# Performance work log

Measured on AMD Instinct MI355X. Metric: run time of the kernel, lower is better.

## Reference

```python
import jax, jax.numpy as jnp
import numpy as np

B, T, C, H = 2, 2048, 1024, 16
D = C // H  # head dim = 64
EPS = 1e-6  # kernel adds 1e-6 to softmax denominator


def setup_inputs() -> dict:
    key = jax.random.key(0)
    k1, k2, k3, k4, k5 = jax.random.split(key, 5)
    s = 1.0 / np.sqrt(C)
    return {
        "x": jax.random.normal(k1, (B, T, C), dtype=jnp.float32),
        "w_attn": jax.random.normal(k2, (3 * C, C), dtype=jnp.float32) * s,
        "b_attn": jax.random.normal(k3, (3 * C,), dtype=jnp.float32) * 0.02,
        "w_proj": jax.random.normal(k4, (C, C), dtype=jnp.float32) * s,
        "b_proj": jax.random.normal(k5, (C,), dtype=jnp.float32) * 0.02,
    }


def reference(x, w_attn, b_attn, w_proj, b_proj):
    b, t, c = x.shape
    qkv = x @ w_attn.T + b_attn                      # [B,T,3C]
    q, k, v = jnp.split(qkv, 3, axis=2)
    # [B,T,C] -> [B,H,T,D]
    q = q.reshape(b, t, H, D).transpose(0, 2, 1, 3)
    k = k.reshape(b, t, H, D).transpose(0, 2, 1, 3)
    v = v.reshape(b, t, H, D).transpose(0, 2, 1, 3)
    scale = 1.0 / np.sqrt(D)
    att = jnp.einsum("bhid,bhjd->bhij", q, k) * scale  # [B,H,T,T]
    causal = jnp.tril(jnp.ones((t, t), dtype=bool))
    att = jnp.where(causal, att, -jnp.inf)
    # softmax matching the HIP kernel: denom has +1e-6
    m = jnp.max(att, axis=-1, keepdims=True)
    e = jnp.exp(att - m)                             # masked entries -> 0
    p = e / (jnp.sum(e, axis=-1, keepdims=True) + EPS)
    y = jnp.einsum("bhij,bhjd->bhid", p, v)          # [B,H,T,D]
    y = y.transpose(0, 2, 1, 3).reshape(b, t, c)     # [B,T,C]
    return y @ w_proj.T + b_proj
```

## Files before the change

kernel.cpp:

```cpp
#include <hip/hip_runtime.h>

#define B_ 2
#define T_ 2048
#define C_ 1024
#define H_ 16
#define D_ 64

typedef __bf16 bf16x8 __attribute__((ext_vector_type(8)));
typedef float f32x4 __attribute__((ext_vector_type(4)));

__device__ __forceinline__ unsigned short f2bf(float f) {
  unsigned u = __float_as_uint(f);
  unsigned r = (u + 0x7fffu + ((u >> 16) & 1u)) >> 16;
  return (unsigned short)r;
}

#define NX 1048576
#define NWA 786432
#define NWP 262144
__global__ __launch_bounds__(256) void convert_all(
    const float* __restrict__ x, const float* __restrict__ wa,
    const float* __restrict__ wp, unsigned short* __restrict__ xb,
    unsigned short* __restrict__ wab, unsigned short* __restrict__ wpb) {
  int i = blockIdx.x * 256 + threadIdx.x;
  const float* s; unsigned short* d; int j;
  if (i < NX)            { s = x;  d = xb;  j = i; }
  else if (i < NX + NWA) { s = wa; d = wab; j = i - NX; }
  else                   { s = wp; d = wpb; j = i - NX - NWA; }
  float4 v = ((const float4*)s)[j];
  ushort4 u;
  u.x = f2bf(v.x); u.y = f2bf(v.y); u.z = f2bf(v.z); u.w = f2bf(v.w);
  ((ushort4*)d)[j] = u;
}

__global__ __launch_bounds__(256) void gemm_bt(
    const unsigned short* __restrict__ A,
    const unsigned short* __restrict__ Bm,
    const float* __restrict__ bias,
    int M, int N, int K, int mode,
    float* __restrict__ outf,
    unsigned short* __restrict__ qb,
    unsigned short* __restrict__ kb,
    unsigned short* __restrict__ vb) {
  __shared__ unsigned short As[128 * 64];
  __shared__ unsigned short Bs[128 * 64];

  const int tid  = threadIdx.x;
  const int lane = tid & 63;
  const int wave = tid >> 6;
  const int quad = lane >> 4;
  const int l16  = lane & 15;
  const int q4   = quad * 4;

  const int bm = blockIdx.y * 128;
  const int bn = blockIdx.x * 128;
  const int wm = (wave >> 1) * 64;
  const int wn = (wave & 1) * 64;

  f32x4 acc[4][4] = {};

  const int srow8 = lane >> 3;
  const int scol  = ((lane & 7) ^ srow8) * 8;
  const int srow  = wave * 8 + srow8;

  for (int k0 = 0; k0 < K; k0 += 64) {
#pragma unroll
    for (int c = 0; c < 4; ++c) {
      const int r = c * 32 + srow;
      const unsigned short* ga = A  + (size_t)(bm + r) * K + (k0 + scol);
      const unsigned short* gb = Bm + (size_t)(bn + r) * K + (k0 + scol);
      unsigned short* la = &As[(c * 32 + wave * 8) * 64];
      unsigned short* lb = &Bs[(c * 32 + wave * 8) * 64];
      __builtin_amdgcn_global_load_lds(
          (__attribute__((address_space(1))) unsigned int*)ga,
          (__attribute__((address_space(3))) unsigned int*)la, 16, 0, 0);
      __builtin_amdgcn_global_load_lds(
          (__attribute__((address_space(1))) unsigned int*)gb,
          (__attribute__((address_space(3))) unsigned int*)lb, 16, 0, 0);
    }
    __syncthreads();
#pragma unroll
    for (int ks = 0; ks < 2; ++ks) {
      bf16x8 af[4], bfr[4];
#pragma unroll
      for (int i = 0; i < 4; ++i)
        af[i] = *(const bf16x8*)&As[(wm + i * 16 + l16) * 64 +
                                    (((ks * 4 + quad) ^ (l16 & 7)) * 8)];
#pragma unroll
      for (int j = 0; j < 4; ++j)
        bfr[j] = *(const bf16x8*)&Bs[(wn + j * 16 + l16) * 64 +
                                     (((ks * 4 + quad) ^ (l16 & 7)) * 8)];
#pragma unroll
      for (int i = 0; i < 4; ++i)
#pragma unroll
        for (int j = 0; j < 4; ++j)
          acc[i][j] = __builtin_amdgcn_mfma_f32_16x16x32_bf16(af[i], bfr[j], acc[i][j], 0, 0, 0);
    }
    __syncthreads();
  }

#pragma unroll
  for (int j = 0; j < 4; ++j) {
    const int gn = bn + wn + j * 16 + l16;
    const float bv = bias[gn];
    if (mode == 0) {
#pragma unroll
      for (int i = 0; i < 4; ++i)
#pragma unroll
        for (int r = 0; r < 4; ++r) {
          const int gm = bm + wm + i * 16 + q4 + r;
          outf[(size_t)gm * N + gn] = acc[i][j][r] + bv;
        }
    } else {
      const int which = gn >> 10;
      const int cc = gn & 1023;
      const int h = cc >> 6, d = cc & 63;
      if (which == 2) {
#pragma unroll
        for (int i = 0; i < 4; ++i) {
          const int gm0 = bm + wm + i * 16 + q4;
          const int b = gm0 >> 11, t0 = gm0 & 2047;
          ushort4 u;
          u.x = f2bf(acc[i][j][0] + bv);
          u.y = f2bf(acc[i][j][1] + bv);
          u.z = f2bf(acc[i][j][2] + bv);
          u.w = f2bf(acc[i][j][3] + bv);
          *(ushort4*)&vb[(((size_t)(b * H_ + h) * D_) + d) * T_ + t0] = u;
        }
      } else {
        const float sc = (which == 0) ? 0.125f : 1.0f;
        unsigned short* dst = (which == 0) ? qb : kb;
#pragma unroll
        for (int i = 0; i < 4; ++i)
#pragma unroll
          for (int r = 0; r < 4; ++r) {
            const int gm = bm + wm + i * 16 + q4 + r;
            const int b = gm >> 11, t = gm & 2047;
            dst[(((size_t)(b * H_ + h) * T_) + t) * D_ + d] = f2bf((acc[i][j][r] + bv) * sc);
          }
      }
    }
  }
}

__global__ __launch_bounds__(256, 3) void attn_mfma(
    const unsigned short* __restrict__ Qb,
    const unsigned short* __restrict__ Kb,
    const unsigned short* __restrict__ Vtg,
    unsigned short* __restrict__ Yb) {
  __shared__ unsigned short Ks[2][64 * 64];
  __shared__ unsigned short Vt[2][64 * 64];
  __shared__ unsigned short Pw[4][32 * 64];

  const int tid  = threadIdx.x;
  const int lane = tid & 63;
  const int wave = tid >> 6;
  const int quad = lane >> 4;
  const int l16  = lane & 15;
  const int q4   = quad * 4;
  const int sw   = (l16 & 7);

  const int id = blockIdx.x;
  int bh, qt;
  if (id < 256) { bh = id & 31; qt = 15 - (id >> 5); }
  else          { bh = (id - 256) & 31; qt = (id - 256) >> 5; }
  const int b = bh >> 4, h = bh & 15;
  const size_t base = (size_t)bh * T_ * D_;

  const int wq = qt * 128 + wave * 32;

  bf16x8 qf[2][2];
#pragma unroll
  for (int nt = 0; nt < 2; ++nt)
#pragma unroll
    for (int ks = 0; ks < 2; ++ks)
      qf[nt][ks] = *(const bf16x8*)(Qb + base + (size_t)(wq + nt * 16 + l16) * 64 +
                                    ks * 32 + quad * 8);

  f32x4 o[4][2] = {};
  float l2[2] = {0.f, 0.f};

  const int ktiles = 2 * qt + 2;
  const int srow8 = lane >> 3;
  const int satom = ((lane & 7) ^ srow8) * 8;

#define STAGE_TILE(KT, BUF)                                                      \
  do {                                                                           \
    const int kt0_ = (KT) * 64;                                                  \
    _Pragma("unroll")                                                            \
    for (int c = 0; c < 2; ++c) {                                                \
      const int row = wave * 16 + c * 8 + srow8;                                 \
      const unsigned short* gk = Kb  + base + (size_t)(kt0_ + row) * 64 + satom; \
      const unsigned short* gv = Vtg + base + (size_t)row * T_ + kt0_ + satom;   \
      __builtin_amdgcn_global_load_lds(                                          \
          (__attribute__((address_space(1))) unsigned int*)gk,                   \
          (__attribute__((address_space(3))) unsigned int*)                      \
              &Ks[BUF][(wave * 16 + c * 8) * 64], 16, 0, 0);                     \
      __builtin_amdgcn_global_load_lds(                                          \
          (__attribute__((address_space(1))) unsigned int*)gv,                   \
          (__attribute__((address_space(3))) unsigned int*)                      \
              &Vt[BUF][(wave * 16 + c * 8) * 64], 16, 0, 0);                     \
    }                                                                            \
  } while (0)

  STAGE_TILE(0, 0);
  __syncthreads();

  for (int kt = 0; kt < ktiles; ++kt) {
    const int kt0 = kt * 64;
    const int cur = kt & 1;
    if (kt + 1 < ktiles) STAGE_TILE(kt + 1, (kt + 1) & 1);

    if (kt0 <= wq + 31) {
      f32x4 s[4][2] = {};
#pragma unroll
      for (int ks = 0; ks < 2; ++ks) {
        bf16x8 kf[4];
#pragma unroll
        for (int mt = 0; mt < 4; ++mt)
          kf[mt] = *(const bf16x8*)&Ks[cur][(mt * 16 + l16) * 64 +
                                           (((ks * 4 + quad) ^ sw) * 8)];
#pragma unroll
        for (int mt = 0; mt < 4; ++mt)
#pragma unroll
          for (int nt = 0; nt < 2; ++nt)
            s[mt][nt] = __builtin_amdgcn_mfma_f32_16x16x32_bf16(kf[mt], qf[nt][ks],
                                                                s[mt][nt], 0, 0, 0);
      }
      if (kt0 + 63 > wq) {
#pragma unroll
        for (int mt = 0; mt < 4; ++mt)
#pragma unroll
          for (int nt = 0; nt < 2; ++nt)
#pragma unroll
            for (int r = 0; r < 4; ++r)
              if (kt0 + mt * 16 + q4 + r > wq + nt * 16 + l16) s[mt][nt][r] = -1e30f;
      }
#pragma unroll
      for (int nt = 0; nt < 2; ++nt) {
        float ps = 0.f;
#pragma unroll
        for (int mt = 0; mt < 4; ++mt) {
          float p0 = __expf(s[mt][nt][0]);
          float p1 = __expf(s[mt][nt][1]);
          float p2 = __expf(s[mt][nt][2]);
          float p3 = __expf(s[mt][nt][3]);
          ps += (p0 + p1) + (p2 + p3);
          unsigned lo = (unsigned)f2bf(p0) | ((unsigned)f2bf(p1) << 16);
          unsigned hi = (unsigned)f2bf(p2) | ((unsigned)f2bf(p3) << 16);
          uint2 pk; pk.x = lo; pk.y = hi;
          const int atom = (2 * mt + (quad >> 1)) ^ sw;
          *(uint2*)&Pw[wave][(nt * 16 + l16) * 64 + atom * 8 + (quad & 1) * 4] = pk;
        }
        l2[nt] += ps;
      }
#pragma unroll
      for (int ks = 0; ks < 2; ++ks) {
        bf16x8 vf[4], pf[2];
#pragma unroll
        for (int dt = 0; dt < 4; ++dt)
          vf[dt] = *(const bf16x8*)&Vt[cur][(dt * 16 + l16) * 64 +
                                           (((ks * 4 + quad) ^ sw) * 8)];
#pragma unroll
        for (int nt = 0; nt < 2; ++nt)
          pf[nt] = *(const bf16x8*)&Pw[wave][(nt * 16 + l16) * 64 +
                                            (((ks * 4 + quad) ^ sw) * 8)];
#pragma unroll
        for (int dt = 0; dt < 4; ++dt)
#pragma unroll
          for (int nt = 0; nt < 2; ++nt)
            o[dt][nt] = __builtin_amdgcn_mfma_f32_16x16x32_bf16(vf[dt], pf[nt],
                                                                o[dt][nt], 0, 0, 0);
      }
    }
    __syncthreads();
  }

#pragma unroll
  for (int nt = 0; nt < 2; ++nt) {
    float l = l2[nt];
    l += __shfl_xor(l, 16);
    l += __shfl_xor(l, 32);
    const float inv = 1.f / (l + 1e-6f);
    const int q = wq + nt * 16 + l16;
#pragma unroll
    for (int dt = 0; dt < 4; ++dt) {
      ushort4 u;
      u.x = f2bf(o[dt][nt][0] * inv);
      u.y = f2bf(o[dt][nt][1] * inv);
      u.z = f2bf(o[dt][nt][2] * inv);
      u.w = f2bf(o[dt][nt][3] * inv);
      *(ushort4*)&Yb[((size_t)(b * T_ + q)) * C_ + h * 64 + dt * 16 + q4] = u;
    }
  }
#undef STAGE_TILE
}

extern "C" void kernel_launch(void* const* d_in, const int* in_sizes, int n_in,
                              void* d_out, int out_size, void* d_ws, size_t ws_size,
                              hipStream_t stream) {
  const float* x      = (const float*)d_in[0];
  const float* w_attn = (const float*)d_in[1];
  const float* b_attn = (const float*)d_in[2];
  const float* w_proj = (const float*)d_in[3];
  const float* b_proj = (const float*)d_in[4];
  float* out = (float*)d_out;

  char* ws = (char*)d_ws;
  unsigned short* xb  = (unsigned short*)ws;  ws += (size_t)4096 * 1024 * 2;
  unsigned short* wab = (unsigned short*)ws;  ws += (size_t)3072 * 1024 * 2;
  unsigned short* wpb = (unsigned short*)ws;  ws += (size_t)1024 * 1024 * 2;
  unsigned short* qb  = (unsigned short*)ws;  ws += (size_t)B_ * H_ * T_ * D_ * 2;
  unsigned short* kb  = (unsigned short*)ws;  ws += (size_t)B_ * H_ * T_ * D_ * 2;
  unsigned short* vb  = (unsigned short*)ws;  ws += (size_t)B_ * H_ * T_ * D_ * 2;
  unsigned short* yb  = (unsigned short*)ws;  ws += (size_t)4096 * 1024 * 2;
  (void)ws_size; (void)in_sizes; (void)n_in; (void)out_size;

  convert_all<<<8192, 256, 0, stream>>>(x, w_attn, w_proj, xb, wab, wpb);

  gemm_bt<<<dim3(24, 32), 256, 0, stream>>>(xb, wab, b_attn, 4096, 3072, 1024, 1,
                                            nullptr, qb, kb, vb);
  attn_mfma<<<512, 256, 0, stream>>>(qb, kb, vb, yb);
  gemm_bt<<<dim3(8, 32), 256, 0, stream>>>(yb, wpb, b_proj, 4096, 1024, 1024, 0,
                                           out, nullptr, nullptr, nullptr);
}
```

Baseline: 189.4 us.

## Load K/V fragments directly into registers per wave, dropping shared-memory staging

Replaces the block-wide LDS double buffering of K and V tiles, together with its per-tile __syncthreads, with per-wave global loads straight into register fragments, double-buffered across two register sets. Each wave now loops only over the key tiles its own causal range needs. The float-to-bf16 packing of P switches to a perm-based round-half-up conversion. In exchange, the four waves of a block each fetch the same K/V data separately, which raises global/L2 traffic. Register pressure also rises, which is why the launch bound is lowered from 3 to 2 blocks per CU.

```diff
diff --git a/kernel.cpp b/kernel.cpp
--- a/kernel.cpp
+++ b/kernel.cpp
@@ -143,13 +143,11 @@
   }
 }
 
-__global__ __launch_bounds__(256, 3) void attn_mfma(
+__global__ __launch_bounds__(256, 2) void attn_mfma(
     const unsigned short* __restrict__ Qb,
     const unsigned short* __restrict__ Kb,
     const unsigned short* __restrict__ Vtg,
     unsigned short* __restrict__ Yb) {
-  __shared__ unsigned short Ks[2][64 * 64];
-  __shared__ unsigned short Vt[2][64 * 64];
   __shared__ unsigned short Pw[4][32 * 64];
 
   const int tid  = threadIdx.x;
@@ -180,101 +178,102 @@
   f32x4 o[4][2] = {};
   float l2[2] = {0.f, 0.f};
 
-  const int ktiles = 2 * qt + 2;
-  const int srow8 = lane >> 3;
-  const int satom = ((lane & 7) ^ srow8) * 8;
-
-#define STAGE_TILE(KT, BUF)                                                      \
-  do {                                                                           \
-    const int kt0_ = (KT) * 64;                                                  \
-    _Pragma("unroll")                                                            \
-    for (int c = 0; c < 2; ++c) {                                                \
-      const int row = wave * 16 + c * 8 + srow8;                                 \
-      const unsigned short* gk = Kb  + base + (size_t)(kt0_ + row) * 64 + satom; \
-      const unsigned short* gv = Vtg + base + (size_t)row * T_ + kt0_ + satom;   \
-      __builtin_amdgcn_global_load_lds(                                          \
-          (__attribute__((address_space(1))) unsigned int*)gk,                   \
-          (__attribute__((address_space(3))) unsigned int*)                      \
-              &Ks[BUF][(wave * 16 + c * 8) * 64], 16, 0, 0);                     \
-      __builtin_amdgcn_global_load_lds(                                          \
-          (__attribute__((address_space(1))) unsigned int*)gv,                   \
-          (__attribute__((address_space(3))) unsigned int*)                      \
-              &Vt[BUF][(wave * 16 + c * 8) * 64], 16, 0, 0);                     \
-    }                                                                            \
+  const int ktiles = (wq + 95) >> 6;
+
+  const unsigned short* kbase = Kb  + base;
+  const unsigned short* vbase = Vtg + base;
+
+  bf16x8 kA[8], vA[8], kB[8], vB[8];
+
+#define LOADK(DST, KT0)                                                         \
+  _Pragma("unroll")                                                             \
+  for (int mt = 0; mt < 4; ++mt)                                                \
+    _Pragma("unroll")                                                           \
+    for (int ks = 0; ks < 2; ++ks)                                              \
+      DST[mt * 2 + ks] = *(const bf16x8*)(kbase +                               \
+          (size_t)((KT0) + mt * 16 + l16) * 64 + ks * 32 + quad * 8);
+#define LOADV(DST, KT0)                                                         \
+  _Pragma("unroll")                                                             \
+  for (int dt = 0; dt < 4; ++dt)                                                \
+    _Pragma("unroll")                                                           \
+    for (int ks = 0; ks < 2; ++ks)                                              \
+      DST[dt * 2 + ks] = *(const bf16x8*)(vbase +                               \
+          (size_t)(dt * 16 + l16) * T_ + (KT0) + ks * 32 + quad * 8);
+
+#define COMPUTE(KF, VF, KT0)                                                    \
+  do {                                                                          \
+    const int kt0_ = (KT0);                                                     \
+    f32x4 s[4][2] = {};                                                         \
+    _Pragma("unroll")                                                           \
+    for (int ks = 0; ks < 2; ++ks)                                              \
+      _Pragma("unroll")                                                         \
+      for (int mt = 0; mt < 4; ++mt)                                            \
+        _Pragma("unroll")                                                       \
+        for (int nt = 0; nt < 2; ++nt)                                          \
+          s[mt][nt] = __builtin_amdgcn_mfma_f32_16x16x32_bf16(                  \
+              KF[mt * 2 + ks], qf[nt][ks], s[mt][nt], 0, 0, 0);                 \
+    if (kt0_ + 63 > wq) {                                                       \
+      _Pragma("unroll")                                                         \
+      for (int mt = 0; mt < 4; ++mt)                                            \
+        _Pragma("unroll")                                                       \
+        for (int nt = 0; nt < 2; ++nt)                                          \
+          _Pragma("unroll")                                                     \
+          for (int r = 0; r < 4; ++r)                                           \
+            if (kt0_ + mt * 16 + q4 + r > wq + nt * 16 + l16)                   \
+              s[mt][nt][r] = -1e30f;                                            \
+    }                                                                           \
+    _Pragma("unroll")                                                           \
+    for (int nt = 0; nt < 2; ++nt) {                                            \
+      float ps = 0.f;                                                           \
+      _Pragma("unroll")                                                         \
+      for (int mt = 0; mt < 4; ++mt) {                                          \
+        float p0 = __expf(s[mt][nt][0]);                                        \
+        float p1 = __expf(s[mt][nt][1]);                                        \
+        float p2 = __expf(s[mt][nt][2]);                                        \
+        float p3 = __expf(s[mt][nt][3]);                                        \
+        ps += (p0 + p1) + (p2 + p3);                                            \
+        unsigned lo = __builtin_amdgcn_perm(__float_as_uint(p1) + 0x8000u,      \
+                                           __float_as_uint(p0) + 0x8000u,      \
+                                           0x07060302u);                        \
+        unsigned hi = __builtin_amdgcn_perm(__float_as_uint(p3) + 0x8000u,      \
+                                           __float_as_uint(p2) + 0x8000u,      \
+                                           0x07060302u);                        \
+        uint2 pk; pk.x = lo; pk.y = hi;                                         \
+        const int atom = (2 * mt + (quad >> 1)) ^ sw;                           \
+        *(uint2*)&Pw[wave][(nt * 16 + l16) * 64 + atom * 8 + (quad & 1) * 4] =  \
+            pk;                                                                 \
+      }                                                                         \
+      l2[nt] += ps;                                                             \
+    }                                                                           \
+    _Pragma("unroll")                                                           \
+    for (int ks = 0; ks < 2; ++ks) {                                            \
+      bf16x8 pf[2];                                                             \
+      _Pragma("unroll")                                                         \
+      for (int nt = 0; nt < 2; ++nt)                                            \
+        pf[nt] = *(const bf16x8*)&Pw[wave][(nt * 16 + l16) * 64 +               \
+                                          (((ks * 4 + quad) ^ sw) * 8)];        \
+      _Pragma("unroll")                                                         \
+      for (int dt = 0; dt < 4; ++dt)                                            \
+        _Pragma("unroll")                                                       \
+        for (int nt = 0; nt < 2; ++nt)                                          \
+          o[dt][nt] = __builtin_amdgcn_mfma_f32_16x16x32_bf16(                  \
+              VF[dt * 2 + ks], pf[nt], o[dt][nt], 0, 0, 0);                     \
+    }                                                                           \
   } while (0)
 
-  STAGE_TILE(0, 0);
-  __syncthreads();
-
-  for (int kt = 0; kt < ktiles; ++kt) {
-    const int kt0 = kt * 64;
-    const int cur = kt & 1;
-    if (kt + 1 < ktiles) STAGE_TILE(kt + 1, (kt + 1) & 1);
-
-    if (kt0 <= wq + 31) {
-      f32x4 s[4][2] = {};
-#pragma unroll
-      for (int ks = 0; ks < 2; ++ks) {
-        bf16x8 kf[4];
-#pragma unroll
-        for (int mt = 0; mt < 4; ++mt)
-          kf[mt] = *(const bf16x8*)&Ks[cur][(mt * 16 + l16) * 64 +
-                                           (((ks * 4 + quad) ^ sw) * 8)];
-#pragma unroll
-        for (int mt = 0; mt < 4; ++mt)
-#pragma unroll
-          for (int nt = 0; nt < 2; ++nt)
-            s[mt][nt] = __builtin_amdgcn_mfma_f32_16x16x32_bf16(kf[mt], qf[nt][ks],
-                                                                s[mt][nt], 0, 0, 0);
-      }
-      if (kt0 + 63 > wq) {
-#pragma unroll
-        for (int mt = 0; mt < 4; ++mt)
-#pragma unroll
-          for (int nt = 0; nt < 2; ++nt)
-#pragma unroll
-            for (int r = 0; r < 4; ++r)
-              if (kt0 + mt * 16 + q4 + r > wq + nt * 16 + l16) s[mt][nt][r] = -1e30f;
-      }
-#pragma unroll
-      for (int nt = 0; nt < 2; ++nt) {
-        float ps = 0.f;
-#pragma unroll
-        for (int mt = 0; mt < 4; ++mt) {
-          float p0 = __expf(s[mt][nt][0]);
-          float p1 = __expf(s[mt][nt][1]);
-          float p2 = __expf(s[mt][nt][2]);
-          float p3 = __expf(s[mt][nt][3]);
-          ps += (p0 + p1) + (p2 + p3);
-          unsigned lo = (unsigned)f2bf(p0) | ((unsigned)f2bf(p1) << 16);
-          unsigned hi = (unsigned)f2bf(p2) | ((unsigned)f2bf(p3) << 16);
-          uint2 pk; pk.x = lo; pk.y = hi;
-          const int atom = (2 * mt + (quad >> 1)) ^ sw;
-          *(uint2*)&Pw[wave][(nt * 16 + l16) * 64 + atom * 8 + (quad & 1) * 4] = pk;
-        }
-        l2[nt] += ps;
-      }
-#pragma unroll
-      for (int ks = 0; ks < 2; ++ks) {
-        bf16x8 vf[4], pf[2];
-#pragma unroll
-        for (int dt = 0; dt < 4; ++dt)
-          vf[dt] = *(const bf16x8*)&Vt[cur][(dt * 16 + l16) * 64 +
-                                           (((ks * 4 + quad) ^ sw) * 8)];
-#pragma unroll
-        for (int nt = 0; nt < 2; ++nt)
-          pf[nt] = *(const bf16x8*)&Pw[wave][(nt * 16 + l16) * 64 +
-                                            (((ks * 4 + quad) ^ sw) * 8)];
-#pragma unroll
-        for (int dt = 0; dt < 4; ++dt)
-#pragma unroll
-          for (int nt = 0; nt < 2; ++nt)
-            o[dt][nt] = __builtin_amdgcn_mfma_f32_16x16x32_bf16(vf[dt], pf[nt],
-                                                                o[dt][nt], 0, 0, 0);
-      }
-    }
-    __syncthreads();
+  LOADK(kA, 0); LOADV(vA, 0);
+  int kt = 0;
+  while (true) {
+    if (kt + 1 < ktiles) { LOADK(kB, (kt + 1) * 64); LOADV(vB, (kt + 1) * 64); }
+    COMPUTE(kA, vA, kt * 64);
+    if (++kt >= ktiles) break;
+    if (kt + 1 < ktiles) { LOADK(kA, (kt + 1) * 64); LOADV(vA, (kt + 1) * 64); }
+    COMPUTE(kB, vB, kt * 64);
+    if (++kt >= ktiles) break;
   }
+#undef LOADK
+#undef LOADV
+#undef COMPUTE
 
 #pragma unroll
   for (int nt = 0; nt < 2; ++nt) {
@@ -293,7 +292,6 @@
       *(ushort4*)&Yb[((size_t)(b * T_ + q)) * C_ + h * 64 + dt * 16 + q4] = u;
     }
   }
-#undef STAGE_TILE
 }
 
 extern "C" void kernel_launch(void* const* d_in, const int* in_sizes, int n_in,
```

Result: slower. 224.8 us (+18.7%).
